# Kernel optimization log

Hardware: AMD Instinct MI355X
Metric: run time of the kernel (lower is better)

Reference implementation:

```python
import jax, jax.numpy as jnp
import numpy as np

N_FEATURE = 12
SIGMA = 0.015
NODES = jnp.linspace(0.0, 0.3, 12)  # RBF centers, matches torch.linspace(0,0.3,12)

B, N, K, FIN = 16, 4096, 32, 4


def setup_inputs() -> dict:
    key = jax.random.key(0)
    ks = jax.random.split(key, 24)

    def make_d(ki, kd):
        idx = jax.random.randint(ki, (B, N, K), 0, N).astype(jnp.float32)
        dist = jax.random.uniform(kd, (B, N, K), minval=0.0, maxval=0.3)
        return jnp.stack([idx, dist], axis=-1)  # [B,N,K,2]

    def lin(kw, kb, fin, fout):
        W = jax.random.normal(kw, (fin, fout), jnp.float32) * (1.0 / np.sqrt(fin))
        b = jax.random.normal(kb, (fout,), jnp.float32) * 0.01
        return W, b

    x = jax.random.normal(ks[0], (B, N, FIN), jnp.float32)
    d1 = make_d(ks[1], ks[2])
    d0 = make_d(ks[3], ks[4])
    dm1 = make_d(ks[5], ks[6])
    mask = jnp.ones((B, N), dtype=bool)

    We, be = lin(ks[7], ks[8], FIN, N_FEATURE)
    Wm1, bm1 = lin(ks[9], ks[10], N_FEATURE + 12, N_FEATURE)
    Wu1, bu1 = lin(ks[11], ks[12], 2 * N_FEATURE, N_FEATURE)
    Wm0, bm0 = lin(ks[13], ks[14], N_FEATURE + 12, N_FEATURE)
    Wu0, bu0 = lin(ks[15], ks[16], 2 * N_FEATURE, N_FEATURE)
    Wmm1, bmm1 = lin(ks[17], ks[18], N_FEATURE + 12, N_FEATURE)
    Wum1, bum1 = lin(ks[19], ks[20], 2 * N_FEATURE, N_FEATURE)

    return {"x": x, "d1": d1, "d0": d0, "dm1": dm1, "mask": mask,
            "We": We, "be": be, "Wm1": Wm1, "bm1": bm1, "Wu1": Wu1, "bu1": bu1,
            "Wm0": Wm0, "bm0": bm0, "Wu0": Wu0, "bu0": bu0,
            "Wmm1": Wmm1, "bmm1": bmm1, "Wum1": Wum1, "bum1": bum1}


def _branch(h, d, Wm, bm, Wu, bu):
    # d: [B,N,K,2] -> channel 0 neighbor index, channel 1 distance
    idx = d[..., 0].astype(jnp.int32)                     # [B,N,K]
    rbf = jnp.exp(-((d[..., 1][..., None] - NODES) ** 2) / (2.0 * SIGMA ** 2))  # [B,N,K,12]
    hj = jax.vmap(lambda hb, ib: hb[ib])(h, idx)          # gather: [B,N,K,F]
    hd = jnp.concatenate([hj, rbf], axis=-1)              # [B,N,K,F+12]
    m = jax.nn.relu(hd @ Wm + bm).sum(axis=2)             # [B,N,F]
    return jax.nn.sigmoid(jnp.concatenate([h, m], axis=-1) @ Wu + bu)  # [B,N,F]


def reference(x, d1, d0, dm1, mask,
              We, be, Wm1, bm1, Wu1, bu1,
              Wm0, bm0, Wu0, bu0,
              Wmm1, bmm1, Wum1, bum1):
    h = jax.nn.relu(x @ We + be)                          # [B,N,12]
    h1 = _branch(h, d1, Wm1, bm1, Wu1, bu1)
    h0 = _branch(h, d0, Wm0, bm0, Wu0, bu0)
    hm1 = _branch(h, dm1, Wmm1, bmm1, Wum1, bum1)
    return (h1, h0, hm1)
```

## Files before the change

kernel.cpp:

```cpp
#include <hip/hip_runtime.h>
#include <hip/hip_fp16.h>
#include <math.h>

#define BBAT 16
#define NNODE 4096
#define KNB 32
#define NF 12
#define TBL 512
#define TMAIN 1024
#define NPB 256
#define CHUNKS 16

#define LDS_BYTES 122880

__device__ __forceinline__ __half2 u2h(unsigned int u) { __half2 h; __builtin_memcpy(&h, &u, 4); return h; }
__device__ __forceinline__ unsigned int h2u(__half2 h) { unsigned int u; __builtin_memcpy(&u, &h, 4); return u; }

__global__ __launch_bounds__(TMAIN) void fused_kernel(
    const float* __restrict__ x, const float* __restrict__ We, const float* __restrict__ be,
    const float* __restrict__ Wm1, const float* __restrict__ bm1,
    const float* __restrict__ Wm0, const float* __restrict__ bm0,
    const float* __restrict__ Wmm1, const float* __restrict__ bmm1,
    const float* __restrict__ d1, const float* __restrict__ d0, const float* __restrict__ dm1,
    const float* __restrict__ Wu1, const float* __restrict__ bu1,
    const float* __restrict__ Wu0, const float* __restrict__ bu0,
    const float* __restrict__ Wum1, const float* __restrict__ bum1,
    float* __restrict__ out)
{
    extern __shared__ char smem[];
    uint2* G0l = (uint2*)smem;
    uint2* G1l = (uint2*)(smem + 32768);
    uint2* G2l = (uint2*)(smem + 65536);
    uint2* A0l = (uint2*)(smem + 98304);
    uint2* A1l = (uint2*)(smem + 102400);
    uint2* A2l = (uint2*)(smem + 106496);
    uint2* A3l = (uint2*)(smem + 110592);
    uint2* A4l = (uint2*)(smem + 114688);
    uint2* A5l = (uint2*)(smem + 118784);

    const int q = blockIdx.x, b = blockIdx.y, br = blockIdx.z;
    const int tid = threadIdx.x;
    const int nl = tid >> 2, sub = tid & 3;
    const int n = q * NPB + nl;
    const size_t slice = (size_t)(br * BBAT + b) * NNODE;

    const float* Wm = (br == 0) ? Wm1 : (br == 1) ? Wm0 : Wmm1;
    const float* bm = (br == 0) ? bm1 : (br == 1) ? bm0 : bmm1;
    const float* dsel = (br == 0) ? d1 : (br == 1) ? d0 : dm1;

    const float4* dp = (const float4*)(dsel + ((size_t)b * NNODE + n) * (size_t)(KNB * 2)) + sub * 4;
    float4 dr0 = dp[0], dr1 = dp[1], dr2 = dp[2], dr3 = dp[3];

    if (tid <= TBL) {
        float dd = (float)tid * (0.3f / (float)TBL);
        float rbf[12];
#pragma unroll
        for (int j = 0; j < 12; j++) {
            float t = dd - (0.3f / 11.0f) * (float)j;
            rbf[j] = expf(-2222.2222222222f * t * t);
        }
        float ph[NF];
#pragma unroll
        for (int c = 0; c < NF; c++) {
            float s = 0.0f;
#pragma unroll
            for (int j = 0; j < 12; j++) s = fmaf(rbf[j], Wm[(12 + j) * NF + c], s);
            ph[c] = s;
        }
        unsigned int c0 = h2u(__floats2half2_rn(ph[0],  ph[1]));
        unsigned int c1 = h2u(__floats2half2_rn(ph[2],  ph[3]));
        unsigned int c2 = h2u(__floats2half2_rn(ph[4],  ph[5]));
        unsigned int c3 = h2u(__floats2half2_rn(ph[6],  ph[7]));
        unsigned int c4 = h2u(__floats2half2_rn(ph[8],  ph[9]));
        unsigned int c5 = h2u(__floats2half2_rn(ph[10], ph[11]));
        if (tid < TBL) {
            A0l[tid] = make_uint2(c0, c1);
            A1l[tid] = make_uint2(c2, c3);
            A2l[tid] = make_uint2(c4, c5);
        }
        if (tid >= 1) {
            A3l[tid - 1] = make_uint2(c0, c1);
            A4l[tid - 1] = make_uint2(c2, c3);
            A5l[tid - 1] = make_uint2(c4, c5);
        }
    }

#pragma unroll
    for (int it = 0; it < 4; it++) {
        const int i = it * TMAIN + tid;
        float4 xv = ((const float4*)x)[(size_t)b * NNODE + i];
        float hv[NF];
#pragma unroll
        for (int f = 0; f < NF; f++) {
            float s = be[f];
            s = fmaf(xv.x, We[0 * NF + f], s);
            s = fmaf(xv.y, We[1 * NF + f], s);
            s = fmaf(xv.z, We[2 * NF + f], s);
            s = fmaf(xv.w, We[3 * NF + f], s);
            hv[f] = fmaxf(s, 0.0f);
        }
        float g[NF];
#pragma unroll
        for (int c = 0; c < NF; c++) {
            float s = bm[c];
#pragma unroll
            for (int j = 0; j < NF; j++) s = fmaf(hv[j], Wm[j * NF + c], s);
            g[c] = s;
        }
        G0l[i] = make_uint2(h2u(__floats2half2_rn(g[0], g[1])),  h2u(__floats2half2_rn(g[2],  g[3])));
        G1l[i] = make_uint2(h2u(__floats2half2_rn(g[4], g[5])),  h2u(__floats2half2_rn(g[6],  g[7])));
        G2l[i] = make_uint2(h2u(__floats2half2_rn(g[8], g[9])),  h2u(__floats2half2_rn(g[10], g[11])));
    }
    __syncthreads();

    int   jv[8];
    float uv[8];
    jv[0] = (int)dr0.x; uv[0] = dr0.y * ((float)TBL / 0.3f);
    jv[1] = (int)dr0.z; uv[1] = dr0.w * ((float)TBL / 0.3f);
    jv[2] = (int)dr1.x; uv[2] = dr1.y * ((float)TBL / 0.3f);
    jv[3] = (int)dr1.z; uv[3] = dr1.w * ((float)TBL / 0.3f);
    jv[4] = (int)dr2.x; uv[4] = dr2.y * ((float)TBL / 0.3f);
    jv[5] = (int)dr2.z; uv[5] = dr2.w * ((float)TBL / 0.3f);
    jv[6] = (int)dr3.x; uv[6] = dr3.y * ((float)TBL / 0.3f);
    jv[7] = (int)dr3.z; uv[7] = dr3.w * ((float)TBL / 0.3f);

    float m[NF];
#pragma unroll
    for (int f = 0; f < NF; f++) m[f] = 0.0f;

#define ACC(O, G, T0, T1) {                                                    \
        __half2 t0 = u2h(T0), t1 = u2h(T1);                                    \
        __half2 phi = __hfma2(f2, __hsub2(t1, t0), t0);                        \
        __half2 s2 = __hadd2(u2h(G), phi);                                     \
        float2 sf = __half22float2(s2);                                        \
        m[O]     += fmaxf(sf.x, 0.0f);                                         \
        m[O + 1] += fmaxf(sf.y, 0.0f);                                         \
    }

#define EDGE(GC0, GC1, GC2, GN0, GN1, GN2, E, PREF)                            \
    {                                                                          \
        if (PREF) { int jn = jv[(E) + 1];                                      \
            GN0 = G0l[jn]; GN1 = G1l[jn]; GN2 = G2l[jn]; }                     \
        float uu = uv[E];                                                      \
        int ii = (int)uu;                                                      \
        ii = min(ii, TBL - 1);                                                 \
        float fr = uu - (float)ii;                                             \
        __half2 f2 = __float2half2_rn(fr);                                     \
        uint2 a0 = A0l[ii], a1 = A1l[ii], a2 = A2l[ii];                        \
        uint2 a3 = A3l[ii], a4 = A4l[ii], a5 = A5l[ii];                        \
        ACC(0,  GC0.x, a0.x, a3.x)                                             \
        ACC(2,  GC0.y, a0.y, a3.y)                                             \
        ACC(4,  GC1.x, a1.x, a4.x)                                             \
        ACC(6,  GC1.y, a1.y, a4.y)                                             \
        ACC(8,  GC2.x, a2.x, a5.x)                                             \
        ACC(10, GC2.y, a2.y, a5.y)                                             \
    }

    uint2 pa0, pa1, pa2, pb0, pb1, pb2;
    { int j0 = jv[0]; pa0 = G0l[j0]; pa1 = G1l[j0]; pa2 = G2l[j0]; }
    EDGE(pa0, pa1, pa2, pb0, pb1, pb2, 0, 1)
    EDGE(pb0, pb1, pb2, pa0, pa1, pa2, 1, 1)
    EDGE(pa0, pa1, pa2, pb0, pb1, pb2, 2, 1)
    EDGE(pb0, pb1, pb2, pa0, pa1, pa2, 3, 1)
    EDGE(pa0, pa1, pa2, pb0, pb1, pb2, 4, 1)
    EDGE(pb0, pb1, pb2, pa0, pa1, pa2, 5, 1)
    EDGE(pa0, pa1, pa2, pb0, pb1, pb2, 6, 1)
    EDGE(pb0, pb1, pb2, pa0, pa1, pa2, 7, 0)

#undef EDGE
#undef ACC

#pragma unroll
    for (int f = 0; f < NF; f++) m[f] += __shfl_xor(m[f], 1);
#pragma unroll
    for (int f = 0; f < NF; f++) m[f] += __shfl_xor(m[f], 2);

    const float* Wu = (br == 0) ? Wu1 : (br == 1) ? Wu0 : Wum1;
    const float* bu = (br == 0) ? bu1 : (br == 1) ? bu0 : bum1;

    float4 xv = ((const float4*)x)[(size_t)b * NNODE + n];
    float hv[NF];
#pragma unroll
    for (int f = 0; f < NF; f++) {
        float s = be[f];
        s = fmaf(xv.x, We[0 * NF + f], s);
        s = fmaf(xv.y, We[1 * NF + f], s);
        s = fmaf(xv.z, We[2 * NF + f], s);
        s = fmaf(xv.w, We[3 * NF + f], s);
        hv[f] = fmaxf(s, 0.0f);
    }

    const int f0 = sub * 3;
    float* op = out + (slice + n) * NF + f0;
#pragma unroll
    for (int ff = 0; ff < 3; ff++) {
        const int f = f0 + ff;
        float a = bu[f];
#pragma unroll
        for (int j = 0; j < NF; j++) a = fmaf(hv[j], Wu[j * NF + f], a);
#pragma unroll
        for (int j = 0; j < NF; j++) a = fmaf(m[j], Wu[(NF + j) * NF + f], a);
        op[ff] = 1.0f / (1.0f + __expf(-a));
    }
}

extern "C" void kernel_launch(void* const* d_in, const int* in_sizes, int n_in,
                              void* d_out, int out_size, void* d_ws, size_t ws_size,
                              hipStream_t stream)
{
    const float* x    = (const float*)d_in[0];
    const float* d1   = (const float*)d_in[1];
    const float* d0   = (const float*)d_in[2];
    const float* dm1  = (const float*)d_in[3];
    const float* We   = (const float*)d_in[5];
    const float* be   = (const float*)d_in[6];
    const float* Wm1  = (const float*)d_in[7];
    const float* bm1  = (const float*)d_in[8];
    const float* Wu1  = (const float*)d_in[9];
    const float* bu1  = (const float*)d_in[10];
    const float* Wm0  = (const float*)d_in[11];
    const float* bm0  = (const float*)d_in[12];
    const float* Wu0  = (const float*)d_in[13];
    const float* bu0  = (const float*)d_in[14];
    const float* Wmm1 = (const float*)d_in[15];
    const float* bmm1 = (const float*)d_in[16];
    const float* Wum1 = (const float*)d_in[17];
    const float* bum1 = (const float*)d_in[18];

    hipFuncSetAttribute((const void*)fused_kernel,
                        hipFuncAttributeMaxDynamicSharedMemorySize, LDS_BYTES);

    fused_kernel<<<dim3(CHUNKS, BBAT, 3), TMAIN, LDS_BYTES, stream>>>(
        x, We, be, Wm1, bm1, Wm0, bm0, Wmm1, bmm1,
        d1, d0, dm1, Wu1, bu1, Wu0, bu0, Wum1, bum1, (float*)d_out);
}
```

Measured before the change: 172.6 us.

## Split per-batch node projection and RBF table into a prep kernel

Adds a prep kernel that computes the per-node message projection g for all three branches, and the RBF lookup tables stored as base plus difference, writing them to workspace. The main kernel then only copies these precomputed arrays into LDS instead of recomputing them in each of the 16 chunk blocks per slice. The interpolation drops one subtraction per element because the differences are stored. Blocks are also reindexed so that blocks for the same slice land on the same XCD, which should improve L2 reuse. The cost is an extra kernel launch and a global write and read of about 4.7 MB.

```diff
diff --git a/kernel.cpp b/kernel.cpp
--- a/kernel.cpp
+++ b/kernel.cpp
@@ -9,18 +9,108 @@
 #define TBL 512
 #define TMAIN 1024
 #define NPB 256
-#define CHUNKS 16
 
 #define LDS_BYTES 122880
 
 __device__ __forceinline__ __half2 u2h(unsigned int u) { __half2 h; __builtin_memcpy(&h, &u, 4); return h; }
 __device__ __forceinline__ unsigned int h2u(__half2 h) { unsigned int u; __builtin_memcpy(&u, &h, 4); return u; }
 
-__global__ __launch_bounds__(TMAIN) void fused_kernel(
+__device__ __forceinline__ void phi_entry(int e, const float* __restrict__ Wm, float* ph)
+{
+    float dd = (float)e * (0.3f / (float)TBL);
+    float rbf[12];
+#pragma unroll
+    for (int j = 0; j < 12; j++) {
+        float t = dd - (0.3f / 11.0f) * (float)j;
+        rbf[j] = expf(-2222.2222222222f * t * t);
+    }
+#pragma unroll
+    for (int c = 0; c < NF; c++) {
+        float s = 0.0f;
+#pragma unroll
+        for (int j = 0; j < 12; j++) s = fmaf(rbf[j], Wm[(12 + j) * NF + c], s);
+        ph[c] = s;
+    }
+}
+
+__global__ __launch_bounds__(256) void prep_kernel(
     const float* __restrict__ x, const float* __restrict__ We, const float* __restrict__ be,
     const float* __restrict__ Wm1, const float* __restrict__ bm1,
     const float* __restrict__ Wm0, const float* __restrict__ bm0,
     const float* __restrict__ Wmm1, const float* __restrict__ bmm1,
+    uint2* __restrict__ gS0, uint2* __restrict__ gS1, uint2* __restrict__ gS2,
+    uint2* __restrict__ T01, uint2* __restrict__ T23, uint2* __restrict__ T45,
+    uint2* __restrict__ D01, uint2* __restrict__ D23, uint2* __restrict__ D45)
+{
+    const int node = blockIdx.x * 256 + threadIdx.x;
+    float4 xv = ((const float4*)x)[node];
+    float hv[NF];
+#pragma unroll
+    for (int f = 0; f < NF; f++) {
+        float s = be[f];
+        s = fmaf(xv.x, We[0 * NF + f], s);
+        s = fmaf(xv.y, We[1 * NF + f], s);
+        s = fmaf(xv.z, We[2 * NF + f], s);
+        s = fmaf(xv.w, We[3 * NF + f], s);
+        hv[f] = fmaxf(s, 0.0f);
+    }
+
+#define DO_G(BR, WM, BM) {                                                     \
+        float g[NF];                                                           \
+        _Pragma("unroll") for (int c = 0; c < NF; c++) {                       \
+            float s = BM[c];                                                   \
+            _Pragma("unroll") for (int j = 0; j < NF; j++)                     \
+                s = fmaf(hv[j], WM[j * NF + c], s);                            \
+            g[c] = s;                                                          \
+        }                                                                      \
+        const size_t o = (size_t)(BR) * 65536 + node;                          \
+        gS0[o] = make_uint2(h2u(__floats2half2_rn(g[0], g[1])),                \
+                            h2u(__floats2half2_rn(g[2], g[3])));               \
+        gS1[o] = make_uint2(h2u(__floats2half2_rn(g[4], g[5])),                \
+                            h2u(__floats2half2_rn(g[6], g[7])));               \
+        gS2[o] = make_uint2(h2u(__floats2half2_rn(g[8], g[9])),                \
+                            h2u(__floats2half2_rn(g[10], g[11])));             \
+    }
+    DO_G(0, Wm1, bm1)
+    DO_G(1, Wm0, bm0)
+    DO_G(2, Wmm1, bmm1)
+#undef DO_G
+
+    if (blockIdx.x < 3) {
+        const int br = blockIdx.x;
+        const float* Wm = (br == 0) ? Wm1 : (br == 1) ? Wm0 : Wmm1;
+        for (int i = threadIdx.x; i < TBL; i += 256) {
+            float p0[NF], p1[NF];
+            phi_entry(i, Wm, p0);
+            phi_entry(i + 1, Wm, p1);
+            __half2 w0 = __floats2half2_rn(p0[0],  p0[1]);
+            __half2 w1 = __floats2half2_rn(p0[2],  p0[3]);
+            __half2 w2 = __floats2half2_rn(p0[4],  p0[5]);
+            __half2 w3 = __floats2half2_rn(p0[6],  p0[7]);
+            __half2 w4 = __floats2half2_rn(p0[8],  p0[9]);
+            __half2 w5 = __floats2half2_rn(p0[10], p0[11]);
+            __half2 v0 = __floats2half2_rn(p1[0],  p1[1]);
+            __half2 v1 = __floats2half2_rn(p1[2],  p1[3]);
+            __half2 v2 = __floats2half2_rn(p1[4],  p1[5]);
+            __half2 v3 = __floats2half2_rn(p1[6],  p1[7]);
+            __half2 v4 = __floats2half2_rn(p1[8],  p1[9]);
+            __half2 v5 = __floats2half2_rn(p1[10], p1[11]);
+            const int o = br * TBL + i;
+            T01[o] = make_uint2(h2u(w0), h2u(w1));
+            T23[o] = make_uint2(h2u(w2), h2u(w3));
+            T45[o] = make_uint2(h2u(w4), h2u(w5));
+            D01[o] = make_uint2(h2u(__hsub2(v0, w0)), h2u(__hsub2(v1, w1)));
+            D23[o] = make_uint2(h2u(__hsub2(v2, w2)), h2u(__hsub2(v3, w3)));
+            D45[o] = make_uint2(h2u(__hsub2(v4, w4)), h2u(__hsub2(v5, w5)));
+        }
+    }
+}
+
+__global__ __launch_bounds__(TMAIN) void main_kernel(
+    const float* __restrict__ x, const float* __restrict__ We, const float* __restrict__ be,
+    const uint2* __restrict__ gS0, const uint2* __restrict__ gS1, const uint2* __restrict__ gS2,
+    const uint2* __restrict__ T01, const uint2* __restrict__ T23, const uint2* __restrict__ T45,
+    const uint2* __restrict__ D01, const uint2* __restrict__ D23, const uint2* __restrict__ D45,
     const float* __restrict__ d1, const float* __restrict__ d0, const float* __restrict__ dm1,
     const float* __restrict__ Wu1, const float* __restrict__ bu1,
     const float* __restrict__ Wu0, const float* __restrict__ bu0,
@@ -28,88 +118,54 @@
     float* __restrict__ out)
 {
     extern __shared__ char smem[];
-    uint2* G0l = (uint2*)smem;
-    uint2* G1l = (uint2*)(smem + 32768);
-    uint2* G2l = (uint2*)(smem + 65536);
-    uint2* A0l = (uint2*)(smem + 98304);
-    uint2* A1l = (uint2*)(smem + 102400);
-    uint2* A2l = (uint2*)(smem + 106496);
-    uint2* A3l = (uint2*)(smem + 110592);
-    uint2* A4l = (uint2*)(smem + 114688);
-    uint2* A5l = (uint2*)(smem + 118784);
-
-    const int q = blockIdx.x, b = blockIdx.y, br = blockIdx.z;
+    uint2* G0l  = (uint2*)smem;
+    uint2* G1l  = (uint2*)(smem + 32768);
+    uint2* G2l  = (uint2*)(smem + 65536);
+    uint2* T01l = (uint2*)(smem + 98304);
+    uint2* T23l = (uint2*)(smem + 102400);
+    uint2* T45l = (uint2*)(smem + 106496);
+    uint2* D01l = (uint2*)(smem + 110592);
+    uint2* D23l = (uint2*)(smem + 114688);
+    uint2* D45l = (uint2*)(smem + 118784);
+
+    const int w = blockIdx.x;
+    const int xcd = w & 7;
+    const int k = w >> 3;
+    const int slice = xcd + 8 * (k >> 4);
+    const int chunk = k & 15;
+    const int br = slice / BBAT;
+    const int b  = slice % BBAT;
+
     const int tid = threadIdx.x;
     const int nl = tid >> 2, sub = tid & 3;
-    const int n = q * NPB + nl;
-    const size_t slice = (size_t)(br * BBAT + b) * NNODE;
-
-    const float* Wm = (br == 0) ? Wm1 : (br == 1) ? Wm0 : Wmm1;
-    const float* bm = (br == 0) ? bm1 : (br == 1) ? bm0 : bmm1;
+    const int n = chunk * NPB + nl;
+
     const float* dsel = (br == 0) ? d1 : (br == 1) ? d0 : dm1;
 
     const float4* dp = (const float4*)(dsel + ((size_t)b * NNODE + n) * (size_t)(KNB * 2)) + sub * 4;
     float4 dr0 = dp[0], dr1 = dp[1], dr2 = dp[2], dr3 = dp[3];
 
-    if (tid <= TBL) {
-        float dd = (float)tid * (0.3f / (float)TBL);
-        float rbf[12];
-#pragma unroll
-        for (int j = 0; j < 12; j++) {
-            float t = dd - (0.3f / 11.0f) * (float)j;
-            rbf[j] = expf(-2222.2222222222f * t * t);
+    {
+        const uint4* s0 = (const uint4*)(gS0 + (size_t)slice * NNODE);
+        const uint4* s1 = (const uint4*)(gS1 + (size_t)slice * NNODE);
+        const uint4* s2 = (const uint4*)(gS2 + (size_t)slice * NNODE);
+        uint4* L0 = (uint4*)G0l; uint4* L1 = (uint4*)G1l; uint4* L2 = (uint4*)G2l;
+#pragma unroll
+        for (int it = 0; it < 2; it++) {
+            const int i = it * TMAIN + tid;
+            L0[i] = s0[i];
+            L1[i] = s1[i];
+            L2[i] = s2[i];
         }
-        float ph[NF];
-#pragma unroll
-        for (int c = 0; c < NF; c++) {
-            float s = 0.0f;
-#pragma unroll
-            for (int j = 0; j < 12; j++) s = fmaf(rbf[j], Wm[(12 + j) * NF + c], s);
-            ph[c] = s;
+        if (tid < TBL) {
+            const int o = br * TBL + tid;
+            T01l[tid] = T01[o];
+            T23l[tid] = T23[o];
+            T45l[tid] = T45[o];
+            D01l[tid] = D01[o];
+            D23l[tid] = D23[o];
+            D45l[tid] = D45[o];
         }
-        unsigned int c0 = h2u(__floats2half2_rn(ph[0],  ph[1]));
-        unsigned int c1 = h2u(__floats2half2_rn(ph[2],  ph[3]));
-        unsigned int c2 = h2u(__floats2half2_rn(ph[4],  ph[5]));
-        unsigned int c3 = h2u(__floats2half2_rn(ph[6],  ph[7]));
-        unsigned int c4 = h2u(__floats2half2_rn(ph[8],  ph[9]));
-        unsigned int c5 = h2u(__floats2half2_rn(ph[10], ph[11]));
-        if (tid < TBL) {
-            A0l[tid] = make_uint2(c0, c1);
-            A1l[tid] = make_uint2(c2, c3);
-            A2l[tid] = make_uint2(c4, c5);
-        }
-        if (tid >= 1) {
-            A3l[tid - 1] = make_uint2(c0, c1);
-            A4l[tid - 1] = make_uint2(c2, c3);
-            A5l[tid - 1] = make_uint2(c4, c5);
-        }
-    }
-
-#pragma unroll
-    for (int it = 0; it < 4; it++) {
-        const int i = it * TMAIN + tid;
-        float4 xv = ((const float4*)x)[(size_t)b * NNODE + i];
-        float hv[NF];
-#pragma unroll
-        for (int f = 0; f < NF; f++) {
-            float s = be[f];
-            s = fmaf(xv.x, We[0 * NF + f], s);
-            s = fmaf(xv.y, We[1 * NF + f], s);
-            s = fmaf(xv.z, We[2 * NF + f], s);
-            s = fmaf(xv.w, We[3 * NF + f], s);
-            hv[f] = fmaxf(s, 0.0f);
-        }
-        float g[NF];
-#pragma unroll
-        for (int c = 0; c < NF; c++) {
-            float s = bm[c];
-#pragma unroll
-            for (int j = 0; j < NF; j++) s = fmaf(hv[j], Wm[j * NF + c], s);
-            g[c] = s;
-        }
-        G0l[i] = make_uint2(h2u(__floats2half2_rn(g[0], g[1])),  h2u(__floats2half2_rn(g[2],  g[3])));
-        G1l[i] = make_uint2(h2u(__floats2half2_rn(g[4], g[5])),  h2u(__floats2half2_rn(g[6],  g[7])));
-        G2l[i] = make_uint2(h2u(__floats2half2_rn(g[8], g[9])),  h2u(__floats2half2_rn(g[10], g[11])));
     }
     __syncthreads();
 
@@ -128,9 +184,8 @@
 #pragma unroll
     for (int f = 0; f < NF; f++) m[f] = 0.0f;
 
-#define ACC(O, G, T0, T1) {                                                    \
-        __half2 t0 = u2h(T0), t1 = u2h(T1);                                    \
-        __half2 phi = __hfma2(f2, __hsub2(t1, t0), t0);                        \
+#define ACC(O, G, T0, DT) {                                                    \
+        __half2 phi = __hfma2(f2, u2h(DT), u2h(T0));                           \
         __half2 s2 = __hadd2(u2h(G), phi);                                     \
         float2 sf = __half22float2(s2);                                        \
         m[O]     += fmaxf(sf.x, 0.0f);                                         \
@@ -146,14 +201,14 @@
         ii = min(ii, TBL - 1);                                                 \
         float fr = uu - (float)ii;                                             \
         __half2 f2 = __float2half2_rn(fr);                                     \
-        uint2 a0 = A0l[ii], a1 = A1l[ii], a2 = A2l[ii];                        \
-        uint2 a3 = A3l[ii], a4 = A4l[ii], a5 = A5l[ii];                        \
-        ACC(0,  GC0.x, a0.x, a3.x)                                             \
-        ACC(2,  GC0.y, a0.y, a3.y)                                             \
-        ACC(4,  GC1.x, a1.x, a4.x)                                             \
-        ACC(6,  GC1.y, a1.y, a4.y)                                             \
-        ACC(8,  GC2.x, a2.x, a5.x)                                             \
-        ACC(10, GC2.y, a2.y, a5.y)                                             \
+        uint2 ta = T01l[ii], tb = T23l[ii], tc = T45l[ii];                     \
+        uint2 da = D01l[ii], db = D23l[ii], dc = D45l[ii];                     \
+        ACC(0,  GC0.x, ta.x, da.x)                                             \
+        ACC(2,  GC0.y, ta.y, da.y)                                             \
+        ACC(4,  GC1.x, tb.x, db.x)                                             \
+        ACC(6,  GC1.y, tb.y, db.y)                                             \
+        ACC(8,  GC2.x, tc.x, dc.x)                                             \
+        ACC(10, GC2.y, tc.y, dc.y)                                             \
     }
 
     uint2 pa0, pa1, pa2, pb0, pb1, pb2;
@@ -191,7 +246,7 @@
     }
 
     const int f0 = sub * 3;
-    float* op = out + (slice + n) * NF + f0;
+    float* op = out + ((size_t)slice * NNODE + n) * NF + f0;
 #pragma unroll
     for (int ff = 0; ff < 3; ff++) {
         const int f = f0 + ff;
@@ -227,10 +282,24 @@
     const float* Wum1 = (const float*)d_in[17];
     const float* bum1 = (const float*)d_in[18];
 
-    hipFuncSetAttribute((const void*)fused_kernel,
+    char* ws = (char*)d_ws;
+    uint2* gS0 = (uint2*)ws;
+    uint2* gS1 = (uint2*)(ws + 1572864);
+    uint2* gS2 = (uint2*)(ws + 3145728);
+    uint2* T01 = (uint2*)(ws + 4718592);
+    uint2* T23 = (uint2*)(ws + 4730880);
+    uint2* T45 = (uint2*)(ws + 4743168);
+    uint2* D01 = (uint2*)(ws + 4755456);
+    uint2* D23 = (uint2*)(ws + 4767744);
+    uint2* D45 = (uint2*)(ws + 4780032);
+
+    hipFuncSetAttribute((const void*)main_kernel,
                         hipFuncAttributeMaxDynamicSharedMemorySize, LDS_BYTES);
 
-    fused_kernel<<<dim3(CHUNKS, BBAT, 3), TMAIN, LDS_BYTES, stream>>>(
+    prep_kernel<<<dim3(256), 256, 0, stream>>>(
         x, We, be, Wm1, bm1, Wm0, bm0, Wmm1, bmm1,
+        gS0, gS1, gS2, T01, T23, T45, D01, D23, D45);
+    main_kernel<<<dim3(768), TMAIN, LDS_BYTES, stream>>>(
+        x, We, be, gS0, gS1, gS2, T01, T23, T45, D01, D23, D45,
         d1, d0, dm1, Wu1, bu1, Wu0, bu0, Wum1, bum1, (float*)d_out);
 }
```

Result: faster. 152.5 us (-11.7%).
